# Optimization experiments

Hardware: AMD Instinct MI355X
Metric: run time of the kernel (lower is better)

Reference implementation:

```python
import jax, jax.numpy as jnp
import numpy as np

N, E = 2048, 6144
DV_IN, DV_OUT = 128, 64
DE_IN, DE_OUT = 16, 16


def setup_inputs() -> dict:
    key = jax.random.key(0)
    ks = jax.random.split(key, 11)
    return {
        "H_v": jax.random.normal(ks[0], (N, DV_IN), jnp.float32),
        "H_e": jax.random.normal(ks[1], (E, DE_IN), jnp.float32),
        "adj_v": jax.random.uniform(ks[2], (N, N), jnp.float32),
        "adj_e": jax.random.uniform(ks[3], (E, E), jnp.float32),
        "T": jax.random.normal(ks[4], (N, E), jnp.float32),
        "W_v": jax.random.normal(ks[5], (DV_IN, DV_OUT), jnp.float32) * (1.0 / np.sqrt(DV_OUT)),
        "b_v": jax.random.normal(ks[6], (DV_OUT,), jnp.float32) * 0.01,
        "p_v": jax.random.normal(ks[7], (1, DE_IN), jnp.float32),
        "W_e": jax.random.normal(ks[8], (DE_IN, DE_OUT), jnp.float32) * (1.0 / np.sqrt(DE_OUT)),
        "b_e": jax.random.normal(ks[9], (DE_OUT,), jnp.float32) * 0.01,
        "p_e": jax.random.normal(ks[10], (1, DV_OUT), jnp.float32),
    }


def reference(H_v, H_e, adj_v, adj_e, T, W_v, b_v, p_v, W_e, b_e, p_e):
    n, e = T.shape
    # ---- node layer (AlternateConvolution, node_layer=True) ----
    d_e = (H_e @ p_v.T)[:, 0]                      # [E] per-edge diag values
    mult1 = (T * d_e[None, :]) @ T.T               # T @ diag(d_e) @ T^T -> [N,N]
    idx_n = jnp.arange(n)
    M1 = mult1.at[idx_n, idx_n].set(1.0)           # eye*1 + (1-eye)*multiplier
    adjusted_Av = M1 * adj_v
    Hv_out = adjusted_Av @ (H_v @ W_v) + b_v       # [N, DV_OUT]
    # ---- edge layer (AlternateConvolution, node_layer=False) ----
    d_v = (Hv_out @ p_e.T)[:, 0]                   # [N] per-node diag values
    mult2 = (T.T * d_v[None, :]) @ T               # T^T @ diag(d_v) @ T -> [E,E]
    idx_e = jnp.arange(e)
    M2 = mult2.at[idx_e, idx_e].set(1.0)
    adjusted_Ae = M2 * adj_e
    norm_Ae = adjusted_Ae / (adjusted_Ae.max(axis=0, keepdims=True) + 1e-10)
    He_out = norm_Ae @ (H_e @ W_e) + b_e           # [E, DE_OUT]
    return Hv_out, He_out
```

## Files before the change

kernel.cpp:

```cpp
#include <hip/hip_runtime.h>

typedef unsigned short u16;
typedef unsigned int u32;
typedef __bf16 bf16x8 __attribute__((ext_vector_type(8)));
typedef float f32x4 __attribute__((ext_vector_type(4)));

#define NN 2048
#define NE 6144
#define DVIN 128
#define DVOUT 64
#define DEIN 16
#define DEOUT 16

#define BM 128
#define BN 128
#define BK 64
#define MS 132

__device__ __forceinline__ u16 f2b(float f) {
  __bf16 b = (__bf16)f;
  return __builtin_bit_cast(u16, b);
}

__device__ __forceinline__ float b2f(u16 u) {
  return __uint_as_float(((u32)u) << 16);
}

__device__ __forceinline__ void async16(const void* g, void* l) {
  __builtin_amdgcn_global_load_lds(
      (const __attribute__((address_space(1))) void*)g,
      (__attribute__((address_space(3))) void*)l, 16, 0, 0);
}

__device__ __forceinline__ bf16x8 load8(const u16* p) {
  union { uint4 u; bf16x8 b; } w;
  w.u = *(const uint4*)p;
  return w.b;
}

__device__ __forceinline__ void tri_decode(int L, int Nt, int& bi, int& bj) {
  float Nf = (float)Nt + 0.5f;
  int b = (int)(Nf - sqrtf(Nf * Nf - 2.0f * (float)L));
  while (b * Nt - (b * (b - 1)) / 2 > L) b--;
  while ((b + 1) * Nt - ((b + 1) * b) / 2 <= L) b++;
  bi = b;
  bj = b + (L - (b * Nt - (b * (b - 1)) / 2));
}


__global__ __launch_bounds__(256) void k_de(const float* __restrict__ He,
                                            const float* __restrict__ pv,
                                            float* __restrict__ de) {
  int j = blockIdx.x * 256 + threadIdx.x;
  float s = 0.f;
#pragma unroll
  for (int k = 0; k < DEIN; k++) s += He[j * DEIN + k] * pv[k];
  de[j] = s;
}

__global__ __launch_bounds__(256) void k_tb(const float* __restrict__ T,
                                            const float* __restrict__ de,
                                            u16* __restrict__ Tb,
                                            u16* __restrict__ Tbs) {
  size_t idx = (size_t)blockIdx.x * 256 + threadIdx.x;
  size_t f = idx * 8;
  float4 v0 = *(const float4*)(T + f);
  float4 v1 = *(const float4*)(T + f + 4);
  int col = (int)(f % (size_t)NE);
  float4 d0 = *(const float4*)(de + col);
  float4 d1 = *(const float4*)(de + col + 4);
  float v[8] = {v0.x, v0.y, v0.z, v0.w, v1.x, v1.y, v1.z, v1.w};
  float d[8] = {d0.x, d0.y, d0.z, d0.w, d1.x, d1.y, d1.z, d1.w};
  union { u16 s[8]; uint4 u; } a, b;
#pragma unroll
  for (int j = 0; j < 8; j++) { a.s[j] = f2b(v[j]); b.s[j] = f2b(v[j] * d[j]); }
  *(uint4*)(Tb + f) = a.u;
  *(uint4*)(Tbs + f) = b.u;
}

__global__ __launch_bounds__(256) void k_x(const float* __restrict__ Hv,
                                           const float* __restrict__ Wv,
                                           u16* __restrict__ Xt) {
  int i = blockIdx.x * 256 + threadIdx.x;
  int d = blockIdx.y;
  float s = 0.f;
#pragma unroll 8
  for (int k = 0; k < DVIN; k++) s += Hv[i * DVIN + k] * Wv[k * DVOUT + d];
  Xt[(size_t)d * NN + i] = f2b(s);
}

__global__ __launch_bounds__(256) void k_dv(const float* __restrict__ HvOut,
                                            const float* __restrict__ pe,
                                            float* __restrict__ dv) {
  int i = blockIdx.x * 256 + threadIdx.x;
  float s = 0.f;
#pragma unroll
  for (int c = 0; c < DVOUT; c++) s += HvOut[i * DVOUT + c] * pe[c];
  dv[i] = s;
}

__global__ __launch_bounds__(256) void k_tt(const float* __restrict__ T,
                                            const float* __restrict__ dv,
                                            u16* __restrict__ Tt,
                                            u16* __restrict__ Tts) {
  __shared__ float tile[32][33];
  int tx = threadIdx.x, ty = threadIdx.y;
  int bx = blockIdx.x, by = blockIdx.y;
  int col = bx * 32 + tx;
#pragma unroll
  for (int r = 0; r < 4; r++) {
    int row = by * 32 + ty + r * 8;
    tile[ty + r * 8][tx] = T[(size_t)row * NE + col];
  }
  __syncthreads();
  int ocol = by * 32 + tx;
  float dvv = dv[ocol];
#pragma unroll
  for (int r = 0; r < 4; r++) {
    int orow = bx * 32 + ty + r * 8;
    float v = tile[tx][ty + r * 8];
    Tt[(size_t)orow * NN + ocol] = f2b(v);
    Tts[(size_t)orow * NN + ocol] = f2b(v * dvv);
  }
}

__global__ __launch_bounds__(256) void k_zt(const float* __restrict__ He,
                                            const float* __restrict__ We,
                                            const u32* __restrict__ colmax,
                                            u16* __restrict__ Ztb) {
  int b = blockIdx.x * 256 + threadIdx.x;
  float h[16];
  const float4* hp = (const float4*)(He + (size_t)b * DEIN);
#pragma unroll
  for (int q = 0; q < 4; q++) {
    float4 t = hp[q];
    h[q * 4 + 0] = t.x; h[q * 4 + 1] = t.y; h[q * 4 + 2] = t.z; h[q * 4 + 3] = t.w;
  }
  float inv = 1.0f / (__uint_as_float(colmax[b]) + 1e-10f);
#pragma unroll
  for (int d = 0; d < DEOUT; d++) {
    float s = 0.f;
#pragma unroll
    for (int k = 0; k < DEIN; k++) s += h[k] * We[k * DEOUT + d];
    Ztb[(size_t)d * NE + b] = f2b(s * inv);
  }
}

__device__ __forceinline__ void tile_loop(const u16* __restrict__ A,
                                          const u16* __restrict__ B,
                                          int bm0, int bn0, int K,
                                          int kbeg, int kend,
                                          u16* As, u16* Bs,
                                          f32x4 (&acc)[4][4]) {
  const int t = threadIdx.x;
  const int lane = t & 63;
  const int lr = lane & 15, kg = lane >> 4;
  const int wave = t >> 6;
  const int wm = (wave >> 1) * 64, wn = (wave & 1) * 64;

  const int arow = t >> 3;
  const int acolsw = (((t & 7) ^ (arow & 7)) * 8);
  const u16* Ag = A + (size_t)(bm0 + arow) * K + acolsw;
  const u16* Bg = B + (size_t)(bn0 + arow) * K + acolsw;
  u16* Al = &As[t * 8];
  u16* Bl = &Bs[t * 8];

  for (int k0 = kbeg; k0 < kend; k0 += BK) {
    __syncthreads();
#pragma unroll
    for (int r = 0; r < 4; r++) {
      async16(Ag + (size_t)(r * 32) * K + k0, Al + r * 32 * BK);
      async16(Bg + (size_t)(r * 32) * K + k0, Bl + r * 32 * BK);
    }
    __syncthreads();
#pragma unroll
    for (int kk = 0; kk < BK; kk += 32) {
      bf16x8 af[4], bf[4];
#pragma unroll
      for (int mi = 0; mi < 4; mi++) {
        int row = wm + mi * 16 + lr;
        int c = (kk >> 3) + kg;
        af[mi] = load8(&As[row * BK + ((c ^ (row & 7)) << 3)]);
      }
#pragma unroll
      for (int ni = 0; ni < 4; ni++) {
        int row = wn + ni * 16 + lr;
        int c = (kk >> 3) + kg;
        bf[ni] = load8(&Bs[row * BK + ((c ^ (row & 7)) << 3)]);
      }
#pragma unroll
      for (int mi = 0; mi < 4; mi++)
#pragma unroll
        for (int ni = 0; ni < 4; ni++)
          acc[mi][ni] = __builtin_amdgcn_mfma_f32_16x16x32_bf16(
              af[mi], bf[ni], acc[mi][ni], 0, 0, 0);
    }
  }
}

__global__ __launch_bounds__(256) void gemm_sym1(const u16* __restrict__ A,
                                                 const u16* __restrict__ B,
                                                 float* __restrict__ P) {
  const int L = blockIdx.x;
  const int z = L / 136, tri = L - z * 136;
  int bi, bj;
  tri_decode(tri, NN / BM, bi, bj);
  __shared__ u16 As[BM * BK];
  __shared__ u16 Bs[BN * BK];
  const int bm0 = bi * BM, bn0 = bj * BN;
  const int kc = NE / 4;
  f32x4 acc[4][4];
#pragma unroll
  for (int i = 0; i < 4; i++)
#pragma unroll
    for (int j = 0; j < 4; j++) acc[i][j] = (f32x4){0.f, 0.f, 0.f, 0.f};

  tile_loop(A, B, bm0, bn0, NE, z * kc, (z + 1) * kc, As, Bs, acc);

  const int t = threadIdx.x;
  f32x4* P4 = (f32x4*)(P + ((size_t)z * 136 + tri) * (BM * BN) + t * 64);
#pragma unroll
  for (int ni = 0; ni < 4; ni++)
#pragma unroll
    for (int mi = 0; mi < 4; mi++) P4[ni * 4 + mi] = acc[mi][ni];
}

__global__ __launch_bounds__(256) void k_comb(const float* __restrict__ P,
                                              const float* __restrict__ adj,
                                              u16* __restrict__ A1) {
  const int tri = blockIdx.x;
  int bi, bj;
  tri_decode(tri, NN / BM, bi, bj);
  __shared__ float tile[128][129];
  const int bm0 = bi * 128, bn0 = bj * 128;
  const int t = threadIdx.x;
  const bool diagb = (bi == bj);
  const int lane = t & 63, lr = lane & 15, kg = lane >> 4;
  const int wave = t >> 6, wm = (wave >> 1) * 64, wn = (wave & 1) * 64;

  const f32x4* P4 = (const f32x4*)(P + (size_t)tri * (BM * BN) + t * 64);
  const size_t SL = (size_t)136 * BM * BN / 4;
#pragma unroll
  for (int ni = 0; ni < 4; ni++) {
#pragma unroll
    for (int mi = 0; mi < 4; mi++) {
      f32x4 s = P4[ni * 4 + mi];
      f32x4 s1 = P4[SL + ni * 4 + mi];
      f32x4 s2 = P4[2 * SL + ni * 4 + mi];
      f32x4 s3 = P4[3 * SL + ni * 4 + mi];
      s = s + s1 + s2 + s3;
      const int cil = wm + mi * 16 + kg * 4;
      const int cjl = wn + ni * 16 + lr;
#pragma unroll
      for (int r = 0; r < 4; r++) tile[cil + r][cjl] = s[r];
    }
  }
  __syncthreads();
  for (int e = t; e < 128 * 32; e += 256) {
    int row = e >> 5, c4 = (e & 31) * 4;
    size_t off = (size_t)(bm0 + row) * NN + bn0 + c4;
    float4 av = *(const float4*)(adj + off);
    float avv[4] = {av.x, av.y, av.z, av.w};
    union { u16 h[4]; uint2 u; } o;
#pragma unroll
    for (int q = 0; q < 4; q++) {
      float sv = tile[row][c4 + q];
      if (diagb && (c4 + q == row)) sv = 1.0f;
      o.h[q] = f2b(sv * avv[q]);
    }
    *(uint2*)(A1 + off) = o.u;
  }
  if (!diagb) {
    for (int e = t; e < 128 * 32; e += 256) {
      int row = e >> 5, c4 = (e & 31) * 4;
      size_t off = (size_t)(bn0 + row) * NN + bm0 + c4;
      float4 av = *(const float4*)(adj + off);
      float avv[4] = {av.x, av.y, av.z, av.w};
      union { u16 h[4]; uint2 u; } o;
#pragma unroll
      for (int q = 0; q < 4; q++) o.h[q] = f2b(tile[c4 + q][row] * avv[q]);
      *(uint2*)(A1 + off) = o.u;
    }
  }
}

__global__ __launch_bounds__(256) void gemm_sym2(const u16* __restrict__ A,
                                                 const u16* __restrict__ B,
                                                 const float* __restrict__ adj,
                                                 u16* __restrict__ C,
                                                 u32* __restrict__ colmax) {
  int bi, bj;
  tri_decode(blockIdx.x, NE / BM, bi, bj);
  __shared__ union {
    struct { u16 As[BM * BK]; u16 Bs[BN * BK]; } s;
    u16 mir[128 * MS];
  } sh;
  __shared__ u32 cmaxN[128];
  __shared__ u32 cmaxM[128];
  const int bm0 = bi * BM, bn0 = bj * BN;
  const int t = threadIdx.x;
  const int N = NE, K = NN;
  const bool diagb = (bi == bj);
  if (t < 128) { cmaxN[t] = 0u; cmaxM[t] = 0u; }

  f32x4 acc[4][4];
#pragma unroll
  for (int i = 0; i < 4; i++)
#pragma unroll
    for (int j = 0; j < 4; j++) acc[i][j] = (f32x4){0.f, 0.f, 0.f, 0.f};

  tile_loop(A, B, bm0, bn0, K, 0, K, sh.s.As, sh.s.Bs, acc);

  const int lane = t & 63, lr = lane & 15, kg = lane >> 4;
  const int wave = t >> 6, wm = (wave >> 1) * 64, wn = (wave & 1) * 64;

  __syncthreads();

#pragma unroll
  for (int ni = 0; ni < 4; ni++) {
    const int cjl = wn + ni * 16 + lr;
    const int cj = bn0 + cjl;
    float cm = 0.f;
#pragma unroll
    for (int mi = 0; mi < 4; mi++) {
#pragma unroll
      for (int r = 0; r < 4; r++) {
        const int cil = wm + mi * 16 + kg * 4 + r;
        const int ci = bm0 + cil;
        float v = acc[mi][ni][r];
        if (ci == cj) v = 1.0f;
        float w = v * adj[(size_t)ci * N + cj];
        C[(size_t)ci * N + cj] = f2b(w);
        cm = fmaxf(cm, w);
        if (!diagb) sh.mir[cjl * MS + cil] = f2b(v);
      }
    }
    atomicMax(&cmaxN[cjl], __float_as_uint(cm));
  }

  if (!diagb) {
    __syncthreads();
    const int rb = t >> 4, cb = (t & 15) * 8;
    float rmax[8];
#pragma unroll
    for (int q = 0; q < 8; q++) rmax[q] = 0.f;
#pragma unroll
    for (int rr = 0; rr < 8; rr++) {
      const int row = rb + rr * 16;
      union { uint2 u; u16 s[4]; } w0, w1;
      w0.u = *(const uint2*)&sh.mir[row * MS + cb];
      w1.u = *(const uint2*)&sh.mir[row * MS + cb + 4];
      float f[8] = {b2f(w0.s[0]), b2f(w0.s[1]), b2f(w0.s[2]), b2f(w0.s[3]),
                    b2f(w1.s[0]), b2f(w1.s[1]), b2f(w1.s[2]), b2f(w1.s[3])};
      const float* ap = adj + (size_t)(bn0 + row) * N + bm0 + cb;
      float4 a0 = *(const float4*)ap;
      float4 a1 = *(const float4*)(ap + 4);
      float a[8] = {a0.x, a0.y, a0.z, a0.w, a1.x, a1.y, a1.z, a1.w};
      union { u16 s[8]; uint4 u; } o;
#pragma unroll
      for (int q = 0; q < 8; q++) {
        float w = f[q] * a[q];
        rmax[q] = fmaxf(rmax[q], w);
        o.s[q] = f2b(w);
      }
      *(uint4*)&C[(size_t)(bn0 + row) * N + bm0 + cb] = o.u;
    }
#pragma unroll
    for (int q = 0; q < 8; q++)
      atomicMax(&cmaxM[cb + q], __float_as_uint(rmax[q]));
  }

  __syncthreads();
  if (t < 128) {
    atomicMax(&colmax[bn0 + t], cmaxN[t]);
    if (!diagb) atomicMax(&colmax[bm0 + t], cmaxM[t]);
  }
}


__global__ __launch_bounds__(512) void k_hv(const u16* __restrict__ A1,
                                            const u16* __restrict__ Xt,
                                            const float* __restrict__ bv,
                                            float* __restrict__ out) {
  __shared__ float red[8 * 1024];
  const int t = threadIdx.x, wave = t >> 6, lane = t & 63;
  const int lr = lane & 15, kg = lane >> 4;
  const int m0 = blockIdx.x * 16;
  const int K = NN;
  f32x4 acc[4];
#pragma unroll
  for (int i = 0; i < 4; i++) acc[i] = (f32x4){0.f, 0.f, 0.f, 0.f};
  const int kbeg = wave * (K / 8), kend = kbeg + (K / 8);
  for (int k = kbeg; k < kend; k += 32) {
    bf16x8 af = load8(&A1[(size_t)(m0 + lr) * K + k + kg * 8]);
#pragma unroll
    for (int ni = 0; ni < 4; ni++) {
      bf16x8 bfr = load8(&Xt[(size_t)(ni * 16 + lr) * K + k + kg * 8]);
      acc[ni] = __builtin_amdgcn_mfma_f32_16x16x32_bf16(af, bfr, acc[ni], 0, 0, 0);
    }
  }
#pragma unroll
  for (int ni = 0; ni < 4; ni++)
#pragma unroll
    for (int r = 0; r < 4; r++)
      red[wave * 1024 + (kg * 4 + r) * 64 + ni * 16 + lr] = acc[ni][r];
  __syncthreads();
#pragma unroll
  for (int q = 0; q < 2; q++) {
    int e = t + 512 * q;
    int row = e >> 6, col = e & 63;
    float v = bv[col];
#pragma unroll
    for (int w = 0; w < 8; w++) v += red[w * 1024 + e];
    out[(size_t)(m0 + row) * DVOUT + col] = v;
  }
}

__global__ __launch_bounds__(512) void k_he(const u16* __restrict__ adjE,
                                            const u16* __restrict__ Ztb,
                                            const float* __restrict__ be,
                                            float* __restrict__ out) {
  __shared__ float red[8 * 256];
  const int t = threadIdx.x, wave = t >> 6, lane = t & 63;
  const int lr = lane & 15, kg = lane >> 4;
  const int m0 = blockIdx.x * 16;
  const int K = NE;
  f32x4 acc = (f32x4){0.f, 0.f, 0.f, 0.f};
  const int kbeg = wave * (K / 8), kend = kbeg + (K / 8);
  for (int k = kbeg; k < kend; k += 32) {
    bf16x8 af = load8(&adjE[(size_t)(m0 + lr) * K + k + kg * 8]);
    bf16x8 bfr = load8(&Ztb[(size_t)lr * K + k + kg * 8]);
    acc = __builtin_amdgcn_mfma_f32_16x16x32_bf16(af, bfr, acc, 0, 0, 0);
  }
#pragma unroll
  for (int r = 0; r < 4; r++)
    red[wave * 256 + (kg * 4 + r) * 16 + lr] = acc[r];
  __syncthreads();
  if (t < 256) {
    int row = t >> 4, col = t & 15;
    float v = be[col];
#pragma unroll
    for (int w = 0; w < 8; w++) v += red[w * 256 + t];
    out[(size_t)(m0 + row) * DEOUT + col] = v;
  }
}

extern "C" void kernel_launch(void* const* d_in, const int* in_sizes, int n_in,
                              void* d_out, int out_size, void* d_ws, size_t ws_size,
                              hipStream_t stream) {
  const float* H_v = (const float*)d_in[0];
  const float* H_e = (const float*)d_in[1];
  const float* adj_v = (const float*)d_in[2];
  const float* adj_e = (const float*)d_in[3];
  const float* T = (const float*)d_in[4];
  const float* W_v = (const float*)d_in[5];
  const float* b_v = (const float*)d_in[6];
  const float* p_v = (const float*)d_in[7];
  const float* W_e = (const float*)d_in[8];
  const float* b_e = (const float*)d_in[9];
  const float* p_e = (const float*)d_in[10];
  float* outHv = (float*)d_out;
  float* outHe = (float*)d_out + NN * DVOUT;

  char* ws = (char*)d_ws;
  u16* Tb   = (u16*)(ws + 0);
  u16* Tbs  = (u16*)(ws + 25165824);
  u16* Tt   = (u16*)(ws + 50331648);
  u16* Tts  = (u16*)(ws + 75497472);
  u16* adjE = (u16*)(ws + 100663296);
  u16* A1   = (u16*)(ws + 176160768);
  u16* Xt   = (u16*)(ws + 184549376);
  u16* Ztb  = (u16*)(ws + 184811520);
  float* de = (float*)(ws + 185008128);
  float* dv = (float*)(ws + 185032704);
  u32* cmax = (u32*)(ws + 185040896);
  float* P = (float*)(ws + 50331648);

  k_de<<<NE / 256, 256, 0, stream>>>(H_e, p_v, de);
  k_tb<<<(NN * (size_t)NE) / 8 / 256, 256, 0, stream>>>(T, de, Tb, Tbs);
  k_x<<<dim3(NN / 256, DVOUT), 256, 0, stream>>>(H_v, W_v, Xt);
  gemm_sym1<<<4 * 136, 256, 0, stream>>>(Tbs, Tb, P);
  k_comb<<<136, 256, 0, stream>>>(P, adj_v, A1);
  k_hv<<<NN / 16, 512, 0, stream>>>(A1, Xt, b_v, outHv);
  k_dv<<<NN / 256, 256, 0, stream>>>(outHv, p_e, dv);
  k_tt<<<dim3(NE / 32, NN / 32), dim3(32, 8), 0, stream>>>(T, dv, Tt, Tts);
  hipMemsetAsync(cmax, 0, NE * sizeof(u32), stream);
  gemm_sym2<<<(NE / BM) * (NE / BM + 1) / 2, 256, 0, stream>>>(
      Tts, Tt, adj_e, adjE, cmax);
  k_zt<<<NE / 256, 256, 0, stream>>>(H_e, W_e, cmax, Ztb);
  k_he<<<NE / 16, 512, 0, stream>>>(adjE, Ztb, b_e, outHe);
}
```

Before: 619.1 us.

## Double-buffer LDS tiles in GEMM loop and remap block order across XCDs

Replaces the single-buffered global-to-LDS tile loop with a two-stage ping-pong pipeline. The next K tile is prefetched asynchronously while MFMAs run on the current one, using explicit vmcnt waits and barriers in place of two __syncthreads per iteration. Block indices in both symmetric GEMM kernels are also permuted so consecutive blocks land on the same XCD, which should improve L2 reuse. This doubles LDS use per block, which may lower occupancy, and relies on hand-written waitcnt accounting for correctness.

```diff
diff --git a/kernel.cpp b/kernel.cpp
--- a/kernel.cpp
+++ b/kernel.cpp
@@ -146,33 +146,50 @@
   }
 }
 
-__device__ __forceinline__ void tile_loop(const u16* __restrict__ A,
-                                          const u16* __restrict__ B,
-                                          int bm0, int bn0, int K,
-                                          int kbeg, int kend,
-                                          u16* As, u16* Bs,
-                                          f32x4 (&acc)[4][4]) {
+__device__ __forceinline__ void tile_loop_pipe(const u16* __restrict__ A,
+                                               const u16* __restrict__ B,
+                                               int bm0, int bn0, int K,
+                                               int kbeg, int kend,
+                                               u16* lds,
+                                               f32x4 (&acc)[4][4]) {
   const int t = threadIdx.x;
   const int lane = t & 63;
   const int lr = lane & 15, kg = lane >> 4;
   const int wave = t >> 6;
   const int wm = (wave >> 1) * 64, wn = (wave & 1) * 64;
 
+  u16* As0 = lds;
+  u16* Bs0 = lds + BM * BK;
+  u16* As1 = lds + 2 * BM * BK;
+  u16* Bs1 = lds + 3 * BM * BK;
+
   const int arow = t >> 3;
   const int acolsw = (((t & 7) ^ (arow & 7)) * 8);
   const u16* Ag = A + (size_t)(bm0 + arow) * K + acolsw;
   const u16* Bg = B + (size_t)(bn0 + arow) * K + acolsw;
-  u16* Al = &As[t * 8];
-  u16* Bl = &Bs[t * 8];
-
+
+#pragma unroll
+  for (int r = 0; r < 4; r++) {
+    async16(Ag + (size_t)(r * 32) * K + kbeg, As0 + t * 8 + r * 32 * BK);
+    async16(Bg + (size_t)(r * 32) * K + kbeg, Bs0 + t * 8 + r * 32 * BK);
+  }
+
+  int cur = 0;
   for (int k0 = kbeg; k0 < kend; k0 += BK) {
-    __syncthreads();
-#pragma unroll
-    for (int r = 0; r < 4; r++) {
-      async16(Ag + (size_t)(r * 32) * K + k0, Al + r * 32 * BK);
-      async16(Bg + (size_t)(r * 32) * K + k0, Bl + r * 32 * BK);
-    }
-    __syncthreads();
+    u16* Ap = cur ? As0 : As1;
+    u16* Bp = cur ? Bs0 : Bs1;
+    const u16* Ac = cur ? As1 : As0;
+    const u16* Bc = cur ? Bs1 : Bs0;
+    if (k0 + BK < kend) {
+#pragma unroll
+      for (int r = 0; r < 4; r++) {
+        async16(Ag + (size_t)(r * 32) * K + k0 + BK, Ap + t * 8 + r * 32 * BK);
+        async16(Bg + (size_t)(r * 32) * K + k0 + BK, Bp + t * 8 + r * 32 * BK);
+      }
+      asm volatile("s_waitcnt vmcnt(8)\n\ts_barrier" ::: "memory");
+    } else {
+      asm volatile("s_waitcnt vmcnt(0)\n\ts_barrier" ::: "memory");
+    }
 #pragma unroll
     for (int kk = 0; kk < BK; kk += 32) {
       bf16x8 af[4], bf[4];
@@ -180,13 +197,13 @@
       for (int mi = 0; mi < 4; mi++) {
         int row = wm + mi * 16 + lr;
         int c = (kk >> 3) + kg;
-        af[mi] = load8(&As[row * BK + ((c ^ (row & 7)) << 3)]);
+        af[mi] = load8(&Ac[row * BK + ((c ^ (row & 7)) << 3)]);
       }
 #pragma unroll
       for (int ni = 0; ni < 4; ni++) {
         int row = wn + ni * 16 + lr;
         int c = (kk >> 3) + kg;
-        bf[ni] = load8(&Bs[row * BK + ((c ^ (row & 7)) << 3)]);
+        bf[ni] = load8(&Bc[row * BK + ((c ^ (row & 7)) << 3)]);
       }
 #pragma unroll
       for (int mi = 0; mi < 4; mi++)
@@ -195,18 +212,20 @@
           acc[mi][ni] = __builtin_amdgcn_mfma_f32_16x16x32_bf16(
               af[mi], bf[ni], acc[mi][ni], 0, 0, 0);
     }
+    asm volatile("s_barrier" ::: "memory");
+    cur ^= 1;
   }
 }
 
 __global__ __launch_bounds__(256) void gemm_sym1(const u16* __restrict__ A,
                                                  const u16* __restrict__ B,
                                                  float* __restrict__ P) {
-  const int L = blockIdx.x;
+  const int L0 = blockIdx.x;
+  const int L = (L0 & 7) * 68 + (L0 >> 3);
   const int z = L / 136, tri = L - z * 136;
   int bi, bj;
   tri_decode(tri, NN / BM, bi, bj);
-  __shared__ u16 As[BM * BK];
-  __shared__ u16 Bs[BN * BK];
+  __shared__ u16 lds[4 * BM * BK];
   const int bm0 = bi * BM, bn0 = bj * BN;
   const int kc = NE / 4;
   f32x4 acc[4][4];
@@ -215,7 +234,7 @@
 #pragma unroll
     for (int j = 0; j < 4; j++) acc[i][j] = (f32x4){0.f, 0.f, 0.f, 0.f};
 
-  tile_loop(A, B, bm0, bn0, NE, z * kc, (z + 1) * kc, As, Bs, acc);
+  tile_loop_pipe(A, B, bm0, bn0, NE, z * kc, (z + 1) * kc, lds, acc);
 
   const int t = threadIdx.x;
   f32x4* P4 = (f32x4*)(P + ((size_t)z * 136 + tri) * (BM * BN) + t * 64);
@@ -289,10 +308,12 @@
                                                  const float* __restrict__ adj,
                                                  u16* __restrict__ C,
                                                  u32* __restrict__ colmax) {
+  const int TB2 = (NE / BM) * (NE / BM + 1) / 2;
+  const int L = (blockIdx.x & 7) * (TB2 / 8) + (blockIdx.x >> 3);
   int bi, bj;
-  tri_decode(blockIdx.x, NE / BM, bi, bj);
+  tri_decode(L, NE / BM, bi, bj);
   __shared__ union {
-    struct { u16 As[BM * BK]; u16 Bs[BN * BK]; } s;
+    u16 buf[4 * BM * BK];
     u16 mir[128 * MS];
   } sh;
   __shared__ u32 cmaxN[128];
@@ -309,7 +330,7 @@
 #pragma unroll
     for (int j = 0; j < 4; j++) acc[i][j] = (f32x4){0.f, 0.f, 0.f, 0.f};
 
-  tile_loop(A, B, bm0, bn0, K, 0, K, sh.s.As, sh.s.Bs, acc);
+  tile_loop_pipe(A, B, bm0, bn0, K, 0, K, sh.buf, acc);
 
   const int lane = t & 63, lr = lane & 15, kg = lane >> 4;
   const int wave = t >> 6, wm = (wave >> 1) * 64, wn = (wave & 1) * 64;
```

Result: no change. 608.1 us (-1.8%).

## Load MFMA fragments directly from global memory and remap block order for L2 locality

Applied to the files above, without the earlier changes.

Replaces the LDS-staged async-copy tile loop with per-wave direct global loads of bf16 fragments into registers, removing shared-memory staging and the two barriers per K step. Both symmetric GEMMs also permute block indices so that consecutive blocks spread across eight groups, likely to match XCD scheduling and improve L2 reuse. Without LDS, each operand row is re-read from global by the two waves that share it, so the kernel depends more on cache hits and on the 16-byte-per-lane strided access pattern. The TB2/8 split assumes the triangular block count divides evenly by 8.

```diff
diff --git a/kernel.cpp b/kernel.cpp
--- a/kernel.cpp
+++ b/kernel.cpp
@@ -14,7 +14,6 @@
 
 #define BM 128
 #define BN 128
-#define BK 64
 #define MS 132
 
 __device__ __forceinline__ u16 f2b(float f) {
@@ -24,12 +23,6 @@
 
 __device__ __forceinline__ float b2f(u16 u) {
   return __uint_as_float(((u32)u) << 16);
-}
-
-__device__ __forceinline__ void async16(const void* g, void* l) {
-  __builtin_amdgcn_global_load_lds(
-      (const __attribute__((address_space(1))) void*)g,
-      (__attribute__((address_space(3))) void*)l, 16, 0, 0);
 }
 
 __device__ __forceinline__ bf16x8 load8(const u16* p) {
@@ -146,67 +139,45 @@
   }
 }
 
-__device__ __forceinline__ void tile_loop(const u16* __restrict__ A,
-                                          const u16* __restrict__ B,
-                                          int bm0, int bn0, int K,
-                                          int kbeg, int kend,
-                                          u16* As, u16* Bs,
-                                          f32x4 (&acc)[4][4]) {
+__device__ __forceinline__ void tile_loop_direct(const u16* __restrict__ A,
+                                                 const u16* __restrict__ B,
+                                                 int bm0, int bn0, int K,
+                                                 int kbeg, int kend,
+                                                 f32x4 (&acc)[4][4]) {
   const int t = threadIdx.x;
   const int lane = t & 63;
   const int lr = lane & 15, kg = lane >> 4;
   const int wave = t >> 6;
   const int wm = (wave >> 1) * 64, wn = (wave & 1) * 64;
 
-  const int arow = t >> 3;
-  const int acolsw = (((t & 7) ^ (arow & 7)) * 8);
-  const u16* Ag = A + (size_t)(bm0 + arow) * K + acolsw;
-  const u16* Bg = B + (size_t)(bn0 + arow) * K + acolsw;
-  u16* Al = &As[t * 8];
-  u16* Bl = &Bs[t * 8];
-
-  for (int k0 = kbeg; k0 < kend; k0 += BK) {
-    __syncthreads();
-#pragma unroll
-    for (int r = 0; r < 4; r++) {
-      async16(Ag + (size_t)(r * 32) * K + k0, Al + r * 32 * BK);
-      async16(Bg + (size_t)(r * 32) * K + k0, Bl + r * 32 * BK);
-    }
-    __syncthreads();
-#pragma unroll
-    for (int kk = 0; kk < BK; kk += 32) {
-      bf16x8 af[4], bf[4];
-#pragma unroll
-      for (int mi = 0; mi < 4; mi++) {
-        int row = wm + mi * 16 + lr;
-        int c = (kk >> 3) + kg;
-        af[mi] = load8(&As[row * BK + ((c ^ (row & 7)) << 3)]);
-      }
-#pragma unroll
-      for (int ni = 0; ni < 4; ni++) {
-        int row = wn + ni * 16 + lr;
-        int c = (kk >> 3) + kg;
-        bf[ni] = load8(&Bs[row * BK + ((c ^ (row & 7)) << 3)]);
-      }
-#pragma unroll
-      for (int mi = 0; mi < 4; mi++)
-#pragma unroll
-        for (int ni = 0; ni < 4; ni++)
-          acc[mi][ni] = __builtin_amdgcn_mfma_f32_16x16x32_bf16(
-              af[mi], bf[ni], acc[mi][ni], 0, 0, 0);
-    }
+  const u16* Ab = A + (size_t)(bm0 + wm + lr) * K + kg * 8;
+  const u16* Bb = B + (size_t)(bn0 + wn + lr) * K + kg * 8;
+  const size_t R16 = (size_t)16 * K;
+
+#pragma unroll 2
+  for (int k = kbeg; k < kend; k += 32) {
+    bf16x8 af[4], bf[4];
+#pragma unroll
+    for (int mi = 0; mi < 4; mi++) af[mi] = load8(Ab + mi * R16 + k);
+#pragma unroll
+    for (int ni = 0; ni < 4; ni++) bf[ni] = load8(Bb + ni * R16 + k);
+#pragma unroll
+    for (int mi = 0; mi < 4; mi++)
+#pragma unroll
+      for (int ni = 0; ni < 4; ni++)
+        acc[mi][ni] = __builtin_amdgcn_mfma_f32_16x16x32_bf16(
+            af[mi], bf[ni], acc[mi][ni], 0, 0, 0);
   }
 }
 
 __global__ __launch_bounds__(256) void gemm_sym1(const u16* __restrict__ A,
                                                  const u16* __restrict__ B,
                                                  float* __restrict__ P) {
-  const int L = blockIdx.x;
+  const int L0 = blockIdx.x;
+  const int L = (L0 & 7) * 68 + (L0 >> 3);
   const int z = L / 136, tri = L - z * 136;
   int bi, bj;
   tri_decode(tri, NN / BM, bi, bj);
-  __shared__ u16 As[BM * BK];
-  __shared__ u16 Bs[BN * BK];
   const int bm0 = bi * BM, bn0 = bj * BN;
   const int kc = NE / 4;
   f32x4 acc[4][4];
@@ -215,7 +186,7 @@
 #pragma unroll
     for (int j = 0; j < 4; j++) acc[i][j] = (f32x4){0.f, 0.f, 0.f, 0.f};
 
-  tile_loop(A, B, bm0, bn0, NE, z * kc, (z + 1) * kc, As, Bs, acc);
+  tile_loop_direct(A, B, bm0, bn0, NE, z * kc, (z + 1) * kc, acc);
 
   const int t = threadIdx.x;
   f32x4* P4 = (f32x4*)(P + ((size_t)z * 136 + tri) * (BM * BN) + t * 64);
@@ -289,12 +260,11 @@
                                                  const float* __restrict__ adj,
                                                  u16* __restrict__ C,
                                                  u32* __restrict__ colmax) {
+  const int TB2 = (NE / BM) * (NE / BM + 1) / 2;
+  const int L = (blockIdx.x & 7) * (TB2 / 8) + (blockIdx.x >> 3);
   int bi, bj;
-  tri_decode(blockIdx.x, NE / BM, bi, bj);
-  __shared__ union {
-    struct { u16 As[BM * BK]; u16 Bs[BN * BK]; } s;
-    u16 mir[128 * MS];
-  } sh;
+  tri_decode(L, NE / BM, bi, bj);
+  __shared__ u16 mir[128 * MS];
   __shared__ u32 cmaxN[128];
   __shared__ u32 cmaxM[128];
   const int bm0 = bi * BM, bn0 = bj * BN;
@@ -309,7 +279,7 @@
 #pragma unroll
     for (int j = 0; j < 4; j++) acc[i][j] = (f32x4){0.f, 0.f, 0.f, 0.f};
 
-  tile_loop(A, B, bm0, bn0, K, 0, K, sh.s.As, sh.s.Bs, acc);
+  tile_loop_direct(A, B, bm0, bn0, K, 0, K, acc);
 
   const int lane = t & 63, lr = lane & 15, kg = lane >> 4;
   const int wave = t >> 6, wm = (wave >> 1) * 64, wn = (wave & 1) * 64;
@@ -332,7 +302,7 @@
         float w = v * adj[(size_t)ci * N + cj];
         C[(size_t)ci * N + cj] = f2b(w);
         cm = fmaxf(cm, w);
-        if (!diagb) sh.mir[cjl * MS + cil] = f2b(v);
+        if (!diagb) mir[cjl * MS + cil] = f2b(v);
       }
     }
     atomicMax(&cmaxN[cjl], __float_as_uint(cm));
@@ -348,8 +318,8 @@
     for (int rr = 0; rr < 8; rr++) {
       const int row = rb + rr * 16;
       union { uint2 u; u16 s[4]; } w0, w1;
-      w0.u = *(const uint2*)&sh.mir[row * MS + cb];
-      w1.u = *(const uint2*)&sh.mir[row * MS + cb + 4];
+      w0.u = *(const uint2*)&mir[row * MS + cb];
+      w1.u = *(const uint2*)&mir[row * MS + cb + 4];
       float f[8] = {b2f(w0.s[0]), b2f(w0.s[1]), b2f(w0.s[2]), b2f(w0.s[3]),
                     b2f(w1.s[0]), b2f(w1.s[1]), b2f(w1.s[2]), b2f(w1.s[3])};
       const float* ap = adj + (size_t)(bn0 + row) * N + bm0 + cb;
```

Result: slower. 914.2 us (+47.7%).

## Shrink symmetric GEMM tiles, swizzle block order, split-K skinny GEMMs with atomics

Applied to the files above, without the earlier changes.

Reduces the triangular GEMM tile sizes (64 for the node-layer product with 3-way split-K, 96 for the edge-layer product) so more blocks run concurrently across the CUs. Block indices are remapped in a strided order to spread work. The two skinny output GEMMs now split K across more blocks and accumulate into outputs prefilled with bias by a new kernel. The aim is better occupancy and load balance, at the cost of less reuse per tile, more partial-sum traffic, per-element LDS atomics in the mirror path, and non-deterministic float atomics.

```diff
diff --git a/kernel.cpp b/kernel.cpp
--- a/kernel.cpp
+++ b/kernel.cpp
@@ -12,10 +12,13 @@
 #define DEIN 16
 #define DEOUT 16
 
-#define BM 128
-#define BN 128
-#define BK 64
-#define MS 132
+#define T2 96
+#define NT2 (NE / T2)
+#define NB2 (NT2 * (NT2 + 1) / 2)
+#define MS2 100
+#define T1 64
+#define NT1 (NN / T1)
+#define NB1 (NT1 * (NT1 + 1) / 2)
 
 __device__ __forceinline__ u16 f2b(float f) {
   __bf16 b = (__bf16)f;
@@ -146,83 +149,83 @@
   }
 }
 
-__device__ __forceinline__ void tile_loop(const u16* __restrict__ A,
-                                          const u16* __restrict__ B,
-                                          int bm0, int bn0, int K,
-                                          int kbeg, int kend,
-                                          u16* As, u16* Bs,
-                                          f32x4 (&acc)[4][4]) {
-  const int t = threadIdx.x;
-  const int lane = t & 63;
+__global__ __launch_bounds__(256) void k_bias(const float* __restrict__ bv,
+                                              const float* __restrict__ be,
+                                              float* __restrict__ outHv,
+                                              float* __restrict__ outHe) {
+  int i = blockIdx.x * 256 + threadIdx.x;
+  if (i < NN * DVOUT) {
+    outHv[i] = bv[i & 63];
+  } else {
+    int j = i - NN * DVOUT;
+    outHe[j] = be[j & 15];
+  }
+}
+
+__global__ __launch_bounds__(256) void gemm_sym1(const u16* __restrict__ A,
+                                                 const u16* __restrict__ B,
+                                                 float* __restrict__ P) {
+  const int Ls = (blockIdx.x & 7) * 198 + (blockIdx.x >> 3);
+  const int z = Ls / NB1, tri = Ls - z * NB1;
+  int bi, bj;
+  tri_decode(tri, NT1, bi, bj);
+  __shared__ u16 As[T1 * 64];
+  __shared__ u16 Bs[T1 * 64];
+  const int bm0 = bi * T1, bn0 = bj * T1;
+  const int t = threadIdx.x, lane = t & 63;
   const int lr = lane & 15, kg = lane >> 4;
   const int wave = t >> 6;
-  const int wm = (wave >> 1) * 64, wn = (wave & 1) * 64;
+  const int wm = (wave >> 1) * 32, wn = (wave & 1) * 32;
+  const int K = NE;
+  const int kbeg = z * 2048, kend = kbeg + 2048;
+
+  f32x4 acc[2][2];
+#pragma unroll
+  for (int i = 0; i < 2; i++)
+#pragma unroll
+    for (int j = 0; j < 2; j++) acc[i][j] = (f32x4){0.f, 0.f, 0.f, 0.f};
 
   const int arow = t >> 3;
   const int acolsw = (((t & 7) ^ (arow & 7)) * 8);
   const u16* Ag = A + (size_t)(bm0 + arow) * K + acolsw;
   const u16* Bg = B + (size_t)(bn0 + arow) * K + acolsw;
-  u16* Al = &As[t * 8];
-  u16* Bl = &Bs[t * 8];
-
-  for (int k0 = kbeg; k0 < kend; k0 += BK) {
+
+  for (int k0 = kbeg; k0 < kend; k0 += 64) {
     __syncthreads();
 #pragma unroll
-    for (int r = 0; r < 4; r++) {
-      async16(Ag + (size_t)(r * 32) * K + k0, Al + r * 32 * BK);
-      async16(Bg + (size_t)(r * 32) * K + k0, Bl + r * 32 * BK);
+    for (int r = 0; r < 2; r++) {
+      async16(Ag + (size_t)(r * 32) * K + k0, As + t * 8 + r * 2048);
+      async16(Bg + (size_t)(r * 32) * K + k0, Bs + t * 8 + r * 2048);
     }
     __syncthreads();
 #pragma unroll
-    for (int kk = 0; kk < BK; kk += 32) {
-      bf16x8 af[4], bf[4];
-#pragma unroll
-      for (int mi = 0; mi < 4; mi++) {
+    for (int kk = 0; kk < 64; kk += 32) {
+      bf16x8 af[2], bf[2];
+#pragma unroll
+      for (int mi = 0; mi < 2; mi++) {
         int row = wm + mi * 16 + lr;
         int c = (kk >> 3) + kg;
-        af[mi] = load8(&As[row * BK + ((c ^ (row & 7)) << 3)]);
+        af[mi] = load8(&As[row * 64 + ((c ^ (row & 7)) << 3)]);
       }
 #pragma unroll
-      for (int ni = 0; ni < 4; ni++) {
+      for (int ni = 0; ni < 2; ni++) {
         int row = wn + ni * 16 + lr;
         int c = (kk >> 3) + kg;
-        bf[ni] = load8(&Bs[row * BK + ((c ^ (row & 7)) << 3)]);
+        bf[ni] = load8(&Bs[row * 64 + ((c ^ (row & 7)) << 3)]);
       }
 #pragma unroll
-      for (int mi = 0; mi < 4; mi++)
-#pragma unroll
-        for (int ni = 0; ni < 4; ni++)
+      for (int mi = 0; mi < 2; mi++)
+#pragma unroll
+        for (int ni = 0; ni < 2; ni++)
           acc[mi][ni] = __builtin_amdgcn_mfma_f32_16x16x32_bf16(
               af[mi], bf[ni], acc[mi][ni], 0, 0, 0);
     }
   }
-}
-
-__global__ __launch_bounds__(256) void gemm_sym1(const u16* __restrict__ A,
-                                                 const u16* __restrict__ B,
-                                                 float* __restrict__ P) {
-  const int L = blockIdx.x;
-  const int z = L / 136, tri = L - z * 136;
-  int bi, bj;
-  tri_decode(tri, NN / BM, bi, bj);
-  __shared__ u16 As[BM * BK];
-  __shared__ u16 Bs[BN * BK];
-  const int bm0 = bi * BM, bn0 = bj * BN;
-  const int kc = NE / 4;
-  f32x4 acc[4][4];
-#pragma unroll
-  for (int i = 0; i < 4; i++)
-#pragma unroll
-    for (int j = 0; j < 4; j++) acc[i][j] = (f32x4){0.f, 0.f, 0.f, 0.f};
-
-  tile_loop(A, B, bm0, bn0, NE, z * kc, (z + 1) * kc, As, Bs, acc);
-
-  const int t = threadIdx.x;
-  f32x4* P4 = (f32x4*)(P + ((size_t)z * 136 + tri) * (BM * BN) + t * 64);
-#pragma unroll
-  for (int ni = 0; ni < 4; ni++)
-#pragma unroll
-    for (int mi = 0; mi < 4; mi++) P4[ni * 4 + mi] = acc[mi][ni];
+  f32x4* P4 = (f32x4*)(P + ((size_t)z * NB1 + tri) * (T1 * T1) + t * 16);
+#pragma unroll
+  for (int ni = 0; ni < 2; ni++)
+#pragma unroll
+    for (int mi = 0; mi < 2; mi++) P4[ni * 2 + mi] = acc[mi][ni];
 }
 
 __global__ __launch_bounds__(256) void k_comb(const float* __restrict__ P,
@@ -230,25 +233,24 @@
                                               u16* __restrict__ A1) {
   const int tri = blockIdx.x;
   int bi, bj;
-  tri_decode(tri, NN / BM, bi, bj);
-  __shared__ float tile[128][129];
-  const int bm0 = bi * 128, bn0 = bj * 128;
+  tri_decode(tri, NT1, bi, bj);
+  __shared__ float tile[T1][T1 + 1];
+  const int bm0 = bi * T1, bn0 = bj * T1;
   const int t = threadIdx.x;
   const bool diagb = (bi == bj);
   const int lane = t & 63, lr = lane & 15, kg = lane >> 4;
-  const int wave = t >> 6, wm = (wave >> 1) * 64, wn = (wave & 1) * 64;
-
-  const f32x4* P4 = (const f32x4*)(P + (size_t)tri * (BM * BN) + t * 64);
-  const size_t SL = (size_t)136 * BM * BN / 4;
-#pragma unroll
-  for (int ni = 0; ni < 4; ni++) {
-#pragma unroll
-    for (int mi = 0; mi < 4; mi++) {
-      f32x4 s = P4[ni * 4 + mi];
-      f32x4 s1 = P4[SL + ni * 4 + mi];
-      f32x4 s2 = P4[2 * SL + ni * 4 + mi];
-      f32x4 s3 = P4[3 * SL + ni * 4 + mi];
-      s = s + s1 + s2 + s3;
+  const int wave = t >> 6, wm = (wave >> 1) * 32, wn = (wave & 1) * 32;
+
+  const f32x4* P4 = (const f32x4*)(P + (size_t)tri * (T1 * T1) + t * 16);
+  const size_t SL = (size_t)NB1 * (T1 * T1) / 4;
+#pragma unroll
+  for (int ni = 0; ni < 2; ni++) {
+#pragma unroll
+    for (int mi = 0; mi < 2; mi++) {
+      f32x4 s = P4[ni * 2 + mi];
+      f32x4 s1 = P4[SL + ni * 2 + mi];
+      f32x4 s2 = P4[2 * SL + ni * 2 + mi];
+      s = s + s1 + s2;
       const int cil = wm + mi * 16 + kg * 4;
       const int cjl = wn + ni * 16 + lr;
 #pragma unroll
@@ -256,30 +258,29 @@
     }
   }
   __syncthreads();
-  for (int e = t; e < 128 * 32; e += 256) {
-    int row = e >> 5, c4 = (e & 31) * 4;
+#pragma unroll
+  for (int q = 0; q < 4; q++) {
+    int idx = t + 256 * q;
+    int row = idx >> 4, c4 = (idx & 15) * 4;
     size_t off = (size_t)(bm0 + row) * NN + bn0 + c4;
     float4 av = *(const float4*)(adj + off);
     float avv[4] = {av.x, av.y, av.z, av.w};
     union { u16 h[4]; uint2 u; } o;
 #pragma unroll
-    for (int q = 0; q < 4; q++) {
-      float sv = tile[row][c4 + q];
-      if (diagb && (c4 + q == row)) sv = 1.0f;
-      o.h[q] = f2b(sv * avv[q]);
+    for (int j = 0; j < 4; j++) {
+      float sv = tile[row][c4 + j];
+      if (diagb && (c4 + j == row)) sv = 1.0f;
+      o.h[j] = f2b(sv * avv[j]);
     }
     *(uint2*)(A1 + off) = o.u;
-  }
-  if (!diagb) {
-    for (int e = t; e < 128 * 32; e += 256) {
-      int row = e >> 5, c4 = (e & 31) * 4;
-      size_t off = (size_t)(bn0 + row) * NN + bm0 + c4;
-      float4 av = *(const float4*)(adj + off);
-      float avv[4] = {av.x, av.y, av.z, av.w};
-      union { u16 h[4]; uint2 u; } o;
-#pragma unroll
-      for (int q = 0; q < 4; q++) o.h[q] = f2b(tile[c4 + q][row] * avv[q]);
-      *(uint2*)(A1 + off) = o.u;
+    if (!diagb) {
+      size_t off2 = (size_t)(bn0 + row) * NN + bm0 + c4;
+      float4 av2 = *(const float4*)(adj + off2);
+      float a2[4] = {av2.x, av2.y, av2.z, av2.w};
+      union { u16 h[4]; uint2 u; } o2;
+#pragma unroll
+      for (int j = 0; j < 4; j++) o2.h[j] = f2b(tile[c4 + j][row] * a2[j]);
+      *(uint2*)(A1 + off2) = o2.u;
     }
   }
 }
@@ -289,50 +290,88 @@
                                                  const float* __restrict__ adj,
                                                  u16* __restrict__ C,
                                                  u32* __restrict__ colmax) {
+  const int L = (blockIdx.x & 7) * (NB2 / 8) + (blockIdx.x >> 3);
   int bi, bj;
-  tri_decode(blockIdx.x, NE / BM, bi, bj);
+  tri_decode(L, NT2, bi, bj);
   __shared__ union {
-    struct { u16 As[BM * BK]; u16 Bs[BN * BK]; } s;
-    u16 mir[128 * MS];
+    u16 buf[2 * T2 * 64];
+    u16 mir[T2 * MS2];
   } sh;
-  __shared__ u32 cmaxN[128];
-  __shared__ u32 cmaxM[128];
-  const int bm0 = bi * BM, bn0 = bj * BN;
-  const int t = threadIdx.x;
-  const int N = NE, K = NN;
+  __shared__ u32 cmaxN[T2];
+  __shared__ u32 cmaxM[T2];
+  const int bm0 = bi * T2, bn0 = bj * T2;
+  const int t = threadIdx.x, lane = t & 63;
+  const int lr = lane & 15, kg = lane >> 4;
+  const int wave = t >> 6;
+  const int wm = (wave >> 1) * 48, wn = (wave & 1) * 48;
+  const int K = NN;
   const bool diagb = (bi == bj);
-  if (t < 128) { cmaxN[t] = 0u; cmaxM[t] = 0u; }
-
-  f32x4 acc[4][4];
-#pragma unroll
-  for (int i = 0; i < 4; i++)
-#pragma unroll
-    for (int j = 0; j < 4; j++) acc[i][j] = (f32x4){0.f, 0.f, 0.f, 0.f};
-
-  tile_loop(A, B, bm0, bn0, K, 0, K, sh.s.As, sh.s.Bs, acc);
-
-  const int lane = t & 63, lr = lane & 15, kg = lane >> 4;
-  const int wave = t >> 6, wm = (wave >> 1) * 64, wn = (wave & 1) * 64;
+  if (t < T2) { cmaxN[t] = 0u; cmaxM[t] = 0u; }
+
+  f32x4 acc[3][3];
+#pragma unroll
+  for (int i = 0; i < 3; i++)
+#pragma unroll
+    for (int j = 0; j < 3; j++) acc[i][j] = (f32x4){0.f, 0.f, 0.f, 0.f};
+
+  u16* As = sh.buf;
+  u16* Bs = sh.buf + T2 * 64;
+  const int arow = t >> 3;
+  const int acolsw = (((t & 7) ^ (arow & 7)) * 8);
+  const u16* Ag = A + (size_t)(bm0 + arow) * K + acolsw;
+  const u16* Bg = B + (size_t)(bn0 + arow) * K + acolsw;
+
+  for (int k0 = 0; k0 < K; k0 += 64) {
+    __syncthreads();
+#pragma unroll
+    for (int r = 0; r < 3; r++) {
+      async16(Ag + (size_t)(r * 32) * K + k0, As + t * 8 + r * 2048);
+      async16(Bg + (size_t)(r * 32) * K + k0, Bs + t * 8 + r * 2048);
+    }
+    __syncthreads();
+#pragma unroll
+    for (int kk = 0; kk < 64; kk += 32) {
+      bf16x8 af[3], bf[3];
+#pragma unroll
+      for (int mi = 0; mi < 3; mi++) {
+        int row = wm + mi * 16 + lr;
+        int c = (kk >> 3) + kg;
+        af[mi] = load8(&As[row * 64 + ((c ^ (row & 7)) << 3)]);
+      }
+#pragma unroll
+      for (int ni = 0; ni < 3; ni++) {
+        int row = wn + ni * 16 + lr;
+        int c = (kk >> 3) + kg;
+        bf[ni] = load8(&Bs[row * 64 + ((c ^ (row & 7)) << 3)]);
+      }
+#pragma unroll
+      for (int mi = 0; mi < 3; mi++)
+#pragma unroll
+        for (int ni = 0; ni < 3; ni++)
+          acc[mi][ni] = __builtin_amdgcn_mfma_f32_16x16x32_bf16(
+              af[mi], bf[ni], acc[mi][ni], 0, 0, 0);
+    }
+  }
 
   __syncthreads();
 
 #pragma unroll
-  for (int ni = 0; ni < 4; ni++) {
+  for (int ni = 0; ni < 3; ni++) {
     const int cjl = wn + ni * 16 + lr;
     const int cj = bn0 + cjl;
     float cm = 0.f;
 #pragma unroll
-    for (int mi = 0; mi < 4; mi++) {
+    for (int mi = 0; mi < 3; mi++) {
 #pragma unroll
       for (int r = 0; r < 4; r++) {
         const int cil = wm + mi * 16 + kg * 4 + r;
         const int ci = bm0 + cil;
         float v = acc[mi][ni][r];
         if (ci == cj) v = 1.0f;
-        float w = v * adj[(size_t)ci * N + cj];
-        C[(size_t)ci * N + cj] = f2b(w);
+        float w = v * adj[(size_t)ci * NE + cj];
+        C[(size_t)ci * NE + cj] = f2b(w);
         cm = fmaxf(cm, w);
-        if (!diagb) sh.mir[cjl * MS + cil] = f2b(v);
+        if (!diagb) sh.mir[cjl * MS2 + cil] = f2b(v);
       }
     }
     atomicMax(&cmaxN[cjl], __float_as_uint(cm));
@@ -340,38 +379,27 @@
 
   if (!diagb) {
     __syncthreads();
-    const int rb = t >> 4, cb = (t & 15) * 8;
-    float rmax[8];
-#pragma unroll
-    for (int q = 0; q < 8; q++) rmax[q] = 0.f;
-#pragma unroll
-    for (int rr = 0; rr < 8; rr++) {
-      const int row = rb + rr * 16;
-      union { uint2 u; u16 s[4]; } w0, w1;
-      w0.u = *(const uint2*)&sh.mir[row * MS + cb];
-      w1.u = *(const uint2*)&sh.mir[row * MS + cb + 4];
-      float f[8] = {b2f(w0.s[0]), b2f(w0.s[1]), b2f(w0.s[2]), b2f(w0.s[3]),
-                    b2f(w1.s[0]), b2f(w1.s[1]), b2f(w1.s[2]), b2f(w1.s[3])};
-      const float* ap = adj + (size_t)(bn0 + row) * N + bm0 + cb;
-      float4 a0 = *(const float4*)ap;
-      float4 a1 = *(const float4*)(ap + 4);
-      float a[8] = {a0.x, a0.y, a0.z, a0.w, a1.x, a1.y, a1.z, a1.w};
-      union { u16 s[8]; uint4 u; } o;
-#pragma unroll
-      for (int q = 0; q < 8; q++) {
-        float w = f[q] * a[q];
-        rmax[q] = fmaxf(rmax[q], w);
-        o.s[q] = f2b(w);
+#pragma unroll
+    for (int q = 0; q < 9; q++) {
+      int idx = t + 256 * q;
+      int row = idx / 24, c4 = (idx - row * 24) * 4;
+      union { uint2 u; u16 s[4]; } wv;
+      wv.u = *(const uint2*)&sh.mir[row * MS2 + c4];
+      float4 av = *(const float4*)&adj[(size_t)(bn0 + row) * NE + bm0 + c4];
+      float a[4] = {av.x, av.y, av.z, av.w};
+      union { u16 h[4]; uint2 u; } o;
+#pragma unroll
+      for (int j = 0; j < 4; j++) {
+        float w = b2f(wv.s[j]) * a[j];
+        o.h[j] = f2b(w);
+        atomicMax(&cmaxM[c4 + j], __float_as_uint(w));
       }
-      *(uint4*)&C[(size_t)(bn0 + row) * N + bm0 + cb] = o.u;
-    }
-#pragma unroll
-    for (int q = 0; q < 8; q++)
-      atomicMax(&cmaxM[cb + q], __float_as_uint(rmax[q]));
+      *(uint2*)&C[(size_t)(bn0 + row) * NE + bm0 + c4] = o.u;
+    }
   }
 
   __syncthreads();
-  if (t < 128) {
+  if (t < T2) {
     atomicMax(&colmax[bn0 + t], cmaxN[t]);
     if (!diagb) atomicMax(&colmax[bm0 + t], cmaxM[t]);
   }
@@ -380,17 +408,17 @@
 
 __global__ __launch_bounds__(512) void k_hv(const u16* __restrict__ A1,
                                             const u16* __restrict__ Xt,
-                                            const float* __restrict__ bv,
                                             float* __restrict__ out) {
   __shared__ float red[8 * 1024];
   const int t = threadIdx.x, wave = t >> 6, lane = t & 63;
   const int lr = lane & 15, kg = lane >> 4;
-  const int m0 = blockIdx.x * 16;
+  const int bx = blockIdx.x;
+  const int m0 = (bx & 127) * 16, z = bx >> 7;
   const int K = NN;
   f32x4 acc[4];
 #pragma unroll
   for (int i = 0; i < 4; i++) acc[i] = (f32x4){0.f, 0.f, 0.f, 0.f};
-  const int kbeg = wave * (K / 8), kend = kbeg + (K / 8);
+  const int kbeg = z * 512 + wave * 64, kend = kbeg + 64;
   for (int k = kbeg; k < kend; k += 32) {
     bf16x8 af = load8(&A1[(size_t)(m0 + lr) * K + k + kg * 8]);
 #pragma unroll
@@ -409,24 +437,24 @@
   for (int q = 0; q < 2; q++) {
     int e = t + 512 * q;
     int row = e >> 6, col = e & 63;
-    float v = bv[col];
+    float v = 0.f;
 #pragma unroll
     for (int w = 0; w < 8; w++) v += red[w * 1024 + e];
-    out[(size_t)(m0 + row) * DVOUT + col] = v;
+    atomicAdd(&out[(size_t)(m0 + row) * DVOUT + col], v);
   }
 }
 
 __global__ __launch_bounds__(512) void k_he(const u16* __restrict__ adjE,
                                             const u16* __restrict__ Ztb,
-                                            const float* __restrict__ be,
                                             float* __restrict__ out) {
   __shared__ float red[8 * 256];
   const int t = threadIdx.x, wave = t >> 6, lane = t & 63;
   const int lr = lane & 15, kg = lane >> 4;
-  const int m0 = blockIdx.x * 16;
+  const int bx = blockIdx.x;
+  const int m0 = (bx % 384) * 16, z = bx / 384;
   const int K = NE;
   f32x4 acc = (f32x4){0.f, 0.f, 0.f, 0.f};
-  const int kbeg = wave * (K / 8), kend = kbeg + (K / 8);
+  const int kbeg = z * 3072 + wave * 384, kend = kbeg + 384;
   for (int k = kbeg; k < kend; k += 32) {
     bf16x8 af = load8(&adjE[(size_t)(m0 + lr) * K + k + kg * 8]);
     bf16x8 bfr = load8(&Ztb[(size_t)lr * K + k + kg * 8]);
@@ -438,10 +466,10 @@
   __syncthreads();
   if (t < 256) {
     int row = t >> 4, col = t & 15;
-    float v = be[col];
+    float v = 0.f;
 #pragma unroll
     for (int w = 0; w < 8; w++) v += red[w * 256 + t];
-    out[(size_t)(m0 + row) * DEOUT + col] = v;
+    atomicAdd(&out[(size_t)(m0 + row) * DEOUT + col], v);
   }
 }
 
@@ -479,14 +507,14 @@
   k_de<<<NE / 256, 256, 0, stream>>>(H_e, p_v, de);
   k_tb<<<(NN * (size_t)NE) / 8 / 256, 256, 0, stream>>>(T, de, Tb, Tbs);
   k_x<<<dim3(NN / 256, DVOUT), 256, 0, stream>>>(H_v, W_v, Xt);
-  gemm_sym1<<<4 * 136, 256, 0, stream>>>(Tbs, Tb, P);
-  k_comb<<<136, 256, 0, stream>>>(P, adj_v, A1);
-  k_hv<<<NN / 16, 512, 0, stream>>>(A1, Xt, b_v, outHv);
+  gemm_sym1<<<3 * NB1, 256, 0, stream>>>(Tbs, Tb, P);
+  k_comb<<<NB1, 256, 0, stream>>>(P, adj_v, A1);
+  k_bias<<<(NN * DVOUT + NE * DEOUT) / 256, 256, 0, stream>>>(b_v, b_e, outHv, outHe);
+  k_hv<<<512, 512, 0, stream>>>(A1, Xt, outHv);
   k_dv<<<NN / 256, 256, 0, stream>>>(outHv, p_e, dv);
   k_tt<<<dim3(NE / 32, NN / 32), dim3(32, 8), 0, stream>>>(T, dv, Tt, Tts);
   hipMemsetAsync(cmax, 0, NE * sizeof(u32), stream);
-  gemm_sym2<<<(NE / BM) * (NE / BM + 1) / 2, 256, 0, stream>>>(
-      Tts, Tt, adj_e, adjE, cmax);
+  gemm_sym2<<<NB2, 256, 0, stream>>>(Tts, Tt, adj_e, adjE, cmax);
   k_zt<<<NE / 256, 256, 0, stream>>>(H_e, W_e, cmax, Ztb);
-  k_he<<<NE / 16, 512, 0, stream>>>(adjE, Ztb, b_e, outHe);
-}
+  k_he<<<768, 512, 0, stream>>>(adjE, Ztb, outHe);
+}
```

Result: faster. 563.9 us (-8.9%).
